# Kernel optimization log

Hardware: AMD Instinct MI355X
Metric: run time of the kernel (lower is better)

Reference implementation:

```python
import jax, jax.numpy as jnp
import numpy as np


def setup_inputs() -> dict:
    key = jax.random.key(0)
    kq, kk, kv = jax.random.split(key, 3)
    B, H, S, D = 2, 16, 2048, 128
    q = jax.random.normal(kq, (B, H, S, D), dtype=jnp.float32)
    k = jax.random.normal(kk, (B, H, S, D), dtype=jnp.float32)
    v = jax.random.normal(kv, (B, H, S, D), dtype=jnp.float32)
    return {"q": q, "k": k, "v": v}


def reference(q, k, v):
    # qk: [B,H,S,S] full score matrix (faithful to the naive torch module)
    qk = jnp.einsum("bhsd,bhtd->bhst", q, k)
    m = jnp.max(qk, axis=-1, keepdims=True)          # row max
    p = jnp.exp(qk - m)                               # unnormalized probs
    # NOTE: original module computes lse but returns only the UNNORMALIZED o.
    o = jnp.einsum("bhst,bhtd->bhsd", p, v)
    return o
```

## Files before the change

### kernel.cpp

```cpp
#include <hip/hip_runtime.h>

typedef _Float16 f16x8  __attribute__((ext_vector_type(8)));
typedef _Float16 f16x4  __attribute__((ext_vector_type(4)));
typedef _Float16 f16x2  __attribute__((ext_vector_type(2)));
typedef float    f32x4  __attribute__((ext_vector_type(4)));
typedef float    f32x16 __attribute__((ext_vector_type(16)));
typedef int      i32x2  __attribute__((ext_vector_type(2)));

#define MFMA32(a, b, c) __builtin_amdgcn_mfma_f32_32x32x16_f16((a), (b), (c), 0, 0, 0)

static constexpr int SEQ   = 2048;
static constexpr int DIM   = 128;
static constexpr int QBLK  = 128;
static constexpr int KVBLK = 32;
static constexpr int NKT   = SEQ / KVBLK;
static constexpr int BH    = 2 * 16;
static constexpr int KSTR  = 136;
static constexpr int VSTR  = 40;

__global__ __launch_bounds__(256, 2)
void fa_fwd_kernel(const float* __restrict__ Qg, const float* __restrict__ Kg,
                   const float* __restrict__ Vg, float* __restrict__ Og)
{
    __shared__ __align__(16) _Float16 Ksh[2][KVBLK * KSTR];
    __shared__ __align__(16) _Float16 Vt[2][DIM * VSTR];

    const int tid  = threadIdx.x;
    const int wv   = tid >> 6;
    const int lane = tid & 63;
    const int lq   = lane & 31;
    const int lh   = lane >> 5;

    const int bi = blockIdx.x;
    const int bh = (bi & 7) + 8 * (bi >> 7);
    const int qt = (bi >> 3) & 15;

    const size_t base = (size_t)bh * SEQ * DIM;
    const float* Qp = Qg + base;
    const float* Kp = Kg + base;
    const float* Vp = Vg + base;
    float*       Op = Og + base;

    const int q0 = qt * QBLK + wv * 32;

    constexpr float LOG2E = 1.44269504088896340736f;
    f16x8 qh[8];
    {
        const float* qs = Qp + (size_t)(q0 + lq) * DIM + 8 * lh;
#pragma unroll
        for (int t = 0; t < 8; ++t) {
            const float4 a = *(const float4*)(qs + 16 * t);
            const float4 b = *(const float4*)(qs + 16 * t + 4);
            float xs[8] = {a.x, a.y, a.z, a.w, b.x, b.y, b.z, b.w};
            f16x8 h;
#pragma unroll
            for (int e = 0; e < 8; ++e) h[e] = (_Float16)(xs[e] * LOG2E);
            qh[t] = h;
        }
    }

    f32x16 acc[4];
#pragma unroll
    for (int a = 0; a < 4; ++a)
#pragma unroll
        for (int r = 0; r < 16; ++r) acc[a][r] = 0.0f;

    float mrow  = -3.0e38f;
    float mtrue = -3.0e38f;

    const int ksr = tid >> 3, kc0 = (tid & 7) * 16;
    const int vc  = tid & 31;
    const int vk  = (tid >> 5) * 4;
    const float* kb = Kp + (size_t)ksr * DIM + kc0;
    const float* vb = Vp + (size_t)vk * DIM + vc;

    float4 kreg[4];
    float  vreg[4][4];

    auto stage = [&](int b) {
#pragma unroll
        for (int g = 0; g < 2; ++g) {
            float xs[8] = {kreg[2*g].x, kreg[2*g].y, kreg[2*g].z, kreg[2*g].w,
                           kreg[2*g+1].x, kreg[2*g+1].y, kreg[2*g+1].z, kreg[2*g+1].w};
            f16x8 h;
#pragma unroll
            for (int e = 0; e < 8; ++e) h[e] = (_Float16)xs[e];
            *(f16x8*)((char*)&Ksh[b][0] + (ksr * KSTR + kc0 + 8 * g) * 2) = h;
        }
#pragma unroll
        for (int j = 0; j < 4; ++j) {
            const int d = vc + 32 * j;
            f16x4 tv = {(_Float16)vreg[j][0], (_Float16)vreg[j][1],
                        (_Float16)vreg[j][2], (_Float16)vreg[j][3]};
            *(f16x4*)((char*)&Vt[b][0] + (d * VSTR + vk) * 2) = tv;
        }
    };
    auto loadT = [&](int t) {
        const float* ks_ = kb + (size_t)t * KVBLK * DIM;
        const float* vs_ = vb + (size_t)t * KVBLK * DIM;
#pragma unroll
        for (int u = 0; u < 4; ++u) kreg[u] = *(const float4*)(ks_ + u * 4);
#pragma unroll
        for (int j = 0; j < 4; ++j)
#pragma unroll
            for (int r = 0; r < 4; ++r) vreg[j][r] = vs_[(size_t)r * DIM + 32 * j];
    };

    loadT(0);
    stage(0);
    loadT(1);

    for (int kt = 0; kt < NKT; ++kt) {
        const int cur = kt & 1;
        __syncthreads();

        if (kt + 1 < NKT) stage(cur ^ 1);
        if (kt + 2 < NKT) loadT(kt + 2);
        __builtin_amdgcn_sched_barrier(0);

        const char* Kc = (const char*)&Ksh[cur][0];
        const char* Vc = (const char*)&Vt[cur][0];
        f32x16 s0, s1;
#pragma unroll
        for (int r = 0; r < 16; ++r) { s0[r] = 0.0f; s1[r] = 0.0f; }
        __builtin_amdgcn_s_setprio(1);
#pragma unroll
        for (int t = 0; t < 4; ++t) {
            f16x8 ka = *(const f16x8*)(Kc + (lq * KSTR + 32 * t + 8 * lh) * 2);
            f16x8 kc = *(const f16x8*)(Kc + (lq * KSTR + 32 * t + 16 + 8 * lh) * 2);
            s0 = MFMA32(ka, qh[2 * t], s0);
            s1 = MFMA32(kc, qh[2 * t + 1], s1);
        }
        __builtin_amdgcn_s_setprio(0);
        f32x16 st = s0 + s1;

        int pk[8];
#pragma unroll
        for (int i = 0; i < 8; ++i) {
            f16x2 e = {(_Float16)__builtin_exp2f(st[2 * i] - mrow),
                       (_Float16)__builtin_exp2f(st[2 * i + 1] - mrow)};
            pk[i] = __builtin_bit_cast(int, e);
        }

        float tmax = fmaxf(fmaxf(fmaxf(st[0], st[1]), fmaxf(st[2], st[3])),
                           fmaxf(fmaxf(st[4], st[5]), fmaxf(st[6], st[7])));
        tmax = fmaxf(tmax, fmaxf(fmaxf(fmaxf(st[8], st[9]), fmaxf(st[10], st[11])),
                                 fmaxf(fmaxf(st[12], st[13]), fmaxf(st[14], st[15]))));
        tmax = fmaxf(tmax, __shfl_xor(tmax, 32));
        mtrue = fmaxf(mtrue, tmax);

        if (!__all(tmax - mrow <= 6.0f)) {
            const float mn  = fmaxf(mrow, tmax);
            const float scl = __builtin_exp2f(mrow - mn);
            mrow = mn;
#pragma unroll
            for (int a = 0; a < 4; ++a)
#pragma unroll
                for (int r = 0; r < 16; ++r) acc[a][r] *= scl;
#pragma unroll
            for (int i = 0; i < 8; ++i) {
                f16x2 e = {(_Float16)__builtin_exp2f(st[2 * i] - mn),
                           (_Float16)__builtin_exp2f(st[2 * i + 1] - mn)};
                pk[i] = __builtin_bit_cast(int, e);
            }
        }

#pragma unroll
        for (int s = 0; s < 2; ++s) {
            i32x2 w02 = __builtin_amdgcn_permlane32_swap(pk[4*s+0], pk[4*s+2], false, false);
            i32x2 w13 = __builtin_amdgcn_permlane32_swap(pk[4*s+1], pk[4*s+3], false, false);
            union { int i[4]; f16x8 v; } u;
            u.i[0] = w02[0]; u.i[1] = w13[0]; u.i[2] = w02[1]; u.i[3] = w13[1];
            const f16x8 pb = u.v;
            __builtin_amdgcn_s_setprio(1);
#pragma unroll
            for (int dm = 0; dm < 4; ++dm) {
                const int d = dm * 32 + lq;
                f16x8 va = *(const f16x8*)(Vc + (d * VSTR + 16 * s + 8 * lh) * 2);
                acc[dm] = MFMA32(va, pb, acc[dm]);
            }
            __builtin_amdgcn_s_setprio(0);
        }
    }

    const float fin = __builtin_exp2f(mrow - mtrue);
#pragma unroll
    for (int a = 0; a < 4; ++a)
#pragma unroll
        for (int r = 0; r < 16; ++r) acc[a][r] *= fin;

    float* ob = Op + (size_t)(q0 + lq) * DIM + 4 * lh;
#pragma unroll
    for (int dm = 0; dm < 4; ++dm)
#pragma unroll
        for (int kp = 0; kp < 4; ++kp) {
            f32x4 v4 = {acc[dm][4*kp], acc[dm][4*kp+1], acc[dm][4*kp+2], acc[dm][4*kp+3]};
            *(f32x4*)(ob + dm * 32 + kp * 8) = v4;
        }
}

extern "C" void kernel_launch(void* const* d_in, const int* in_sizes, int n_in,
                              void* d_out, int out_size, void* d_ws, size_t ws_size,
                              hipStream_t stream) {
    const float* q = (const float*)d_in[0];
    const float* k = (const float*)d_in[1];
    const float* v = (const float*)d_in[2];
    float* o = (float*)d_out;
    dim3 grid((SEQ / QBLK) * BH);
    fa_fwd_kernel<<<grid, dim3(256), 0, stream>>>(q, k, v, o);
}
```

Measured before the change: 115.0 us.

## Split KV range across two blocks per query tile and merge partial outputs

```diff
diff --git a/kernel.cpp b/kernel.cpp
--- a/kernel.cpp
+++ b/kernel.cpp
@@ -18,9 +18,10 @@
 static constexpr int KSTR  = 136;
 static constexpr int VSTR  = 40;
 
-__global__ __launch_bounds__(256, 2)
+__global__ __launch_bounds__(256, 3)
 void fa_fwd_kernel(const float* __restrict__ Qg, const float* __restrict__ Kg,
-                   const float* __restrict__ Vg, float* __restrict__ Og)
+                   const float* __restrict__ Vg, float* __restrict__ OutA,
+                   float* __restrict__ OutB, float* __restrict__ Mbase, int split)
 {
     __shared__ __align__(16) _Float16 Ksh[2][KVBLK * KSTR];
     __shared__ __align__(16) _Float16 Vt[2][DIM * VSTR];
@@ -32,14 +33,16 @@
     const int lh   = lane >> 5;
 
     const int bi = blockIdx.x;
-    const int bh = (bi & 7) + 8 * (bi >> 7);
-    const int qt = (bi >> 3) & 15;
+    int bh, qt, khalf;
+    if (split) { bh = (bi & 7) + 8 * (bi >> 8); khalf = (bi >> 3) & 1; qt = (bi >> 4) & 15; }
+    else       { bh = (bi & 7) + 8 * (bi >> 7); khalf = 0;             qt = (bi >> 3) & 15; }
+    const int nkt = split ? (NKT / 2) : NKT;
 
     const size_t base = (size_t)bh * SEQ * DIM;
     const float* Qp = Qg + base;
-    const float* Kp = Kg + base;
-    const float* Vp = Vg + base;
-    float*       Op = Og + base;
+    const float* Kp = Kg + base + (size_t)khalf * (SEQ / 2) * DIM;
+    const float* Vp = Vg + base + (size_t)khalf * (SEQ / 2) * DIM;
+    float*       Op = (khalf ? OutB : OutA) + base;
 
     const int q0 = qt * QBLK + wv * 32;
 
@@ -110,12 +113,12 @@
     stage(0);
     loadT(1);
 
-    for (int kt = 0; kt < NKT; ++kt) {
+    for (int kt = 0; kt < nkt; ++kt) {
         const int cur = kt & 1;
         __syncthreads();
 
-        if (kt + 1 < NKT) stage(cur ^ 1);
-        if (kt + 2 < NKT) loadT(kt + 2);
+        if (kt + 1 < nkt) stage(cur ^ 1);
+        if (kt + 2 < nkt) loadT(kt + 2);
         __builtin_amdgcn_sched_barrier(0);
 
         const char* Kc = (const char*)&Ksh[cur][0];
@@ -197,6 +200,28 @@
             f32x4 v4 = {acc[dm][4*kp], acc[dm][4*kp+1], acc[dm][4*kp+2], acc[dm][4*kp+3]};
             *(f32x4*)(ob + dm * 32 + kp * 8) = v4;
         }
+    if (split && lane < 32)
+        Mbase[(size_t)khalf * (BH * SEQ) + (size_t)bh * SEQ + q0 + lq] = mtrue;
+}
+
+__global__ __launch_bounds__(256)
+void fa_merge(float* __restrict__ O0, const float* __restrict__ O1,
+              const float* __restrict__ M)
+{
+    const int idx = blockIdx.x * 256 + threadIdx.x;
+    const int row = idx >> 5;
+    const float m0 = M[row];
+    const float m1 = M[BH * SEQ + row];
+    const float mm = fmaxf(m0, m1);
+    const float s0 = __builtin_exp2f(m0 - mm);
+    const float s1 = __builtin_exp2f(m1 - mm);
+    float4 a = ((const float4*)O0)[idx];
+    const float4 b = ((const float4*)O1)[idx];
+    a.x = a.x * s0 + b.x * s1;
+    a.y = a.y * s0 + b.y * s1;
+    a.z = a.z * s0 + b.z * s1;
+    a.w = a.w * s0 + b.w * s1;
+    ((float4*)O0)[idx] = a;
 }
 
 extern "C" void kernel_launch(void* const* d_in, const int* in_sizes, int n_in,
@@ -206,6 +231,17 @@
     const float* k = (const float*)d_in[1];
     const float* v = (const float*)d_in[2];
     float* o = (float*)d_out;
-    dim3 grid((SEQ / QBLK) * BH);
-    fa_fwd_kernel<<<grid, dim3(256), 0, stream>>>(q, k, v, o);
+
+    const size_t needO1 = (size_t)BH * SEQ * DIM * 4;
+    const size_t needM  = (size_t)2 * BH * SEQ * 4;
+    if (ws_size >= needO1 + needM) {
+        float* O1 = (float*)d_ws;
+        float* M  = (float*)((char*)d_ws + needO1);
+        fa_fwd_kernel<<<dim3(2 * (SEQ / QBLK) * BH), dim3(256), 0, stream>>>(
+            q, k, v, o, O1, M, 1);
+        fa_merge<<<dim3(BH * SEQ * DIM / 4 / 256), dim3(256), 0, stream>>>(o, O1, M);
+    } else {
+        fa_fwd_kernel<<<dim3((SEQ / QBLK) * BH), dim3(256), 0, stream>>>(
+            q, k, v, o, nullptr, nullptr, 0);
+    }
 }
```

After: 256.9 us. 2.23x slower.
